# Optimization experiments

Measured on AMD Instinct MI355X. Metric: run time of the kernel, lower is better.

## Reference

```python
import jax, jax.numpy as jnp
import numpy as np

K_TOP = 2  # module's top-k


def setup_inputs() -> dict:
    key = jax.random.key(0)
    ks = jax.random.split(key, 6)
    s = 0.02
    B, S, H, D = 4, 1024, 2048, 1024
    E_SH, E_RT = 2, 16
    return {
        "x": jax.random.normal(ks[0], (B, S, H), dtype=jnp.float32),
        "Wsh_up": jax.random.normal(ks[1], (E_SH, H, D), dtype=jnp.float32) * s,
        "Wsh_down": jax.random.normal(ks[2], (E_SH, D, H), dtype=jnp.float32) * s,
        "Wrt_up": jax.random.normal(ks[3], (E_RT, H, D), dtype=jnp.float32) * s,
        "Wrt_down": jax.random.normal(ks[4], (E_RT, D, H), dtype=jnp.float32) * s,
        "W_router": jax.random.normal(ks[5], (H, E_RT), dtype=jnp.float32) * s,
    }


def reference(x, Wsh_up, Wsh_down, Wrt_up, Wrt_down, W_router):
    B, S, H = x.shape
    E_rt = Wrt_up.shape[0]
    xt = x.reshape(B * S, H)  # [T,H]

    # shared experts (summed)
    sh_mid = jax.nn.gelu(jnp.einsum('th,ehd->ted', xt, Wsh_up), approximate=False)
    shared_out = jnp.einsum('ted,edh->th', sh_mid, Wsh_down)  # [T,H]

    # router: softmax over all routed experts, then top-k
    probs = jax.nn.softmax(xt @ W_router, axis=-1)  # [T,E]
    top_v, top_i = jax.lax.top_k(probs, K_TOP)  # [T,K]
    # per-token dense gate weights over experts (zero for non-selected)
    gate = jnp.sum(jax.nn.one_hot(top_i, E_rt, dtype=xt.dtype) * top_v[..., None], axis=1)  # [T,E]

    # routed experts: compute all experts densely, combine with sparse gate
    rt_mid = jax.nn.gelu(jnp.einsum('th,ehd->ted', xt, Wrt_up), approximate=False)  # [T,E,D]
    routed_out = jnp.einsum('ted,edh->th', rt_mid * gate[:, :, None], Wrt_down)  # [T,H]

    return (shared_out + routed_out).reshape(B, S, H)
```

## Files before the change

### kernel.cpp

```cpp
#include <hip/hip_runtime.h>
#include <cstdint>
#include <cstddef>

typedef __bf16 bf16_t;
typedef __bf16 bf16x8 __attribute__((ext_vector_type(8)));
typedef float floatx4 __attribute__((ext_vector_type(4)));

static constexpr int T_TOK = 4096;
static constexpr int HDIM  = 2048;
static constexpr int DDIM  = 1024;
static constexpr int ESH   = 2;
static constexpr int ERT   = 16;
static constexpr int NPAIR = 2 * T_TOK;
static constexpr int NPAIR_PAD = NPAIR + 128;

__device__ __forceinline__ float gelu_f(float v) {
  return 0.5f * v * (1.0f + erff(v * 0.70710678118654752440f));
}

__global__ __launch_bounds__(256) void router_kernel(
    const float* __restrict__ x, const float* __restrict__ Wr,
    int* __restrict__ top_e, float* __restrict__ top_w, int* __restrict__ counts)
{
  const int t = blockIdx.x;
  const int tid = threadIdx.x;
  float acc[ERT];
#pragma unroll
  for (int e = 0; e < ERT; ++e) acc[e] = 0.f;
  const float* xr = x + (long)t * HDIM;
  for (int h = tid; h < HDIM; h += 256) {
    const float xv = xr[h];
    const float4* w4 = (const float4*)(Wr + h * ERT);
    const float4 w0 = w4[0], w1 = w4[1], w2 = w4[2], w3 = w4[3];
    acc[0]  += xv * w0.x; acc[1]  += xv * w0.y; acc[2]  += xv * w0.z; acc[3]  += xv * w0.w;
    acc[4]  += xv * w1.x; acc[5]  += xv * w1.y; acc[6]  += xv * w1.z; acc[7]  += xv * w1.w;
    acc[8]  += xv * w2.x; acc[9]  += xv * w2.y; acc[10] += xv * w2.z; acc[11] += xv * w2.w;
    acc[12] += xv * w3.x; acc[13] += xv * w3.y; acc[14] += xv * w3.z; acc[15] += xv * w3.w;
  }
  __shared__ float s[256][ERT + 1];
#pragma unroll
  for (int e = 0; e < ERT; ++e) s[tid][e] = acc[e];
  __syncthreads();
  for (int st = 128; st >= 1; st >>= 1) {
    if (tid < st) {
#pragma unroll
      for (int e = 0; e < ERT; ++e) s[tid][e] += s[tid + st][e];
    }
    __syncthreads();
  }
  if (tid == 0) {
    float l[ERT];
    float mx = -1e30f;
#pragma unroll
    for (int e = 0; e < ERT; ++e) { l[e] = s[0][e]; mx = fmaxf(mx, l[e]); }
    float sum = 0.f;
#pragma unroll
    for (int e = 0; e < ERT; ++e) { l[e] = expf(l[e] - mx); sum += l[e]; }
    const float inv = 1.f / sum;
    float v0 = -1.f, v1 = -1.f; int i0 = 0, i1 = 0;
#pragma unroll
    for (int e = 0; e < ERT; ++e) {
      const float p = l[e] * inv;
      if (p > v0) { v1 = v0; i1 = i0; v0 = p; i0 = e; }
      else if (p > v1) { v1 = p; i1 = e; }
    }
    top_e[2 * t] = i0; top_e[2 * t + 1] = i1;
    top_w[2 * t] = v0; top_w[2 * t + 1] = v1;
    atomicAdd(&counts[i0], 1); atomicAdd(&counts[i1], 1);
  }
}

__global__ void prefix_kernel(const int* __restrict__ counts, int* __restrict__ offsets) {
  if (threadIdx.x == 0) {
    int s = 0;
    for (int e = 0; e < ERT; ++e) { offsets[e] = s; s += counts[e]; }
    offsets[ERT] = s;
  }
}

__global__ __launch_bounds__(256) void scatter_kernel(
    const int* __restrict__ top_e, const float* __restrict__ top_w,
    const int* __restrict__ offsets, int* __restrict__ cursor,
    int* __restrict__ pair_token, float* __restrict__ pair_w)
{
  const int t = blockIdx.x * 256 + threadIdx.x;
  if (t >= T_TOK) return;
#pragma unroll
  for (int k = 0; k < 2; ++k) {
    const int e = top_e[2 * t + k];
    const int pos = atomicAdd(&cursor[e], 1);
    const int slot = offsets[e] + pos;
    pair_token[slot] = t;
    pair_w[slot] = top_w[2 * t + k];
  }
}

__global__ __launch_bounds__(256) void cast_x_kernel(const float* __restrict__ x, bf16_t* __restrict__ xb) {
  const long base = (long)blockIdx.x * HDIM + threadIdx.x * 8;
  const float4 a = *(const float4*)(x + base);
  const float4 b = *(const float4*)(x + base + 4);
  bf16x8 v;
  v[0] = (__bf16)a.x; v[1] = (__bf16)a.y; v[2] = (__bf16)a.z; v[3] = (__bf16)a.w;
  v[4] = (__bf16)b.x; v[5] = (__bf16)b.y; v[6] = (__bf16)b.z; v[7] = (__bf16)b.w;
  *(bf16x8*)(xb + base) = v;
}

__global__ __launch_bounds__(256) void gather_kernel(
    const float* __restrict__ x, const int* __restrict__ pair_token, bf16_t* __restrict__ xg)
{
  const int slot = blockIdx.x;
  const int tok = pair_token[slot];
  const float* src = x + (long)tok * HDIM;
  const int c = threadIdx.x * 8;
  const float4 a = *(const float4*)(src + c);
  const float4 b = *(const float4*)(src + c + 4);
  bf16x8 v;
  v[0] = (__bf16)a.x; v[1] = (__bf16)a.y; v[2] = (__bf16)a.z; v[3] = (__bf16)a.w;
  v[4] = (__bf16)b.x; v[5] = (__bf16)b.y; v[6] = (__bf16)b.z; v[7] = (__bf16)b.w;
  *(bf16x8*)(xg + (long)slot * HDIM + c) = v;
}

__global__ __launch_bounds__(256) void transpose_cast_kernel(
    const float* __restrict__ in, bf16_t* __restrict__ out, int R, int C)
{
  __shared__ float tl[64][65];
  const long mat = blockIdx.z;
  in  += mat * (long)R * C;
  out += mat * (long)R * C;
  const int c0 = blockIdx.x * 64, r0 = blockIdx.y * 64;
  const int tid = threadIdx.x;
  const int lr = tid >> 4;
  const int lc4 = (tid & 15) * 4;
#pragma unroll
  for (int i = 0; i < 4; ++i) {
    const int r = lr + i * 16;
    const float4 v = *(const float4*)(in + (long)(r0 + r) * C + c0 + lc4);
    tl[r][lc4 + 0] = v.x; tl[r][lc4 + 1] = v.y; tl[r][lc4 + 2] = v.z; tl[r][lc4 + 3] = v.w;
  }
  __syncthreads();
#pragma unroll
  for (int i = 0; i < 4; ++i) {
    const int c = lr + i * 16;
    ushort4 o;
    o.x = __builtin_bit_cast(unsigned short, (__bf16)tl[lc4 + 0][c]);
    o.y = __builtin_bit_cast(unsigned short, (__bf16)tl[lc4 + 1][c]);
    o.z = __builtin_bit_cast(unsigned short, (__bf16)tl[lc4 + 2][c]);
    o.w = __builtin_bit_cast(unsigned short, (__bf16)tl[lc4 + 3][c]);
    *(ushort4*)((unsigned short*)out + (long)(c0 + c) * R + r0 + lc4) = o;
  }
}

template<int MODE>
__global__ __launch_bounds__(256) void gemm_kernel(
    const bf16_t* __restrict__ Abase, const bf16_t* __restrict__ Bbase,
    bf16_t* __restrict__ Cbf, float* __restrict__ Cf,
    const int* __restrict__ counts, const int* __restrict__ offsets,
    const float* __restrict__ pair_w, const int* __restrict__ pair_token)
{
  constexpr int K   = (MODE == 3) ? 1024 : 2048;
  constexpr int LDA = (MODE == 3) ? 1024 : 2048;
  constexpr int LDB = (MODE == 1 || MODE == 3) ? 1024 : 2048;

  const int mt = blockIdx.x, nt = blockIdx.y, e = blockIdx.z;
  const int m0 = mt * 128;
  int cnt = 0, segoff = 0;
  if (MODE == 2 || MODE == 3) {
    cnt = counts[e];
    if (m0 >= cnt) return;
    segoff = offsets[e];
  }

  const bf16_t* Ab;
  const bf16_t* Bb;
  if (MODE == 0) {
    Ab = Abase + (long)m0 * LDA;
    Bb = Bbase + (long)(nt >> 3) * ((long)DDIM * HDIM) + (long)((nt & 7) * 128) * LDB;
  } else if (MODE == 1) {
    Ab = Abase + (long)m0 * LDA;
    Bb = Bbase + (long)(nt * 128) * LDB;
  } else if (MODE == 2) {
    Ab = Abase + (long)(segoff + m0) * LDA;
    Bb = Bbase + (long)e * ((long)DDIM * HDIM) + (long)(nt * 128) * LDB;
  } else {
    Ab = Abase + (long)(segoff + m0) * LDA;
    Bb = Bbase + (long)e * ((long)HDIM * DDIM) + (long)(nt * 128) * LDB;
  }

  __shared__ bf16_t As[128 * 72];
  __shared__ bf16_t Bs[128 * 72];

  const int tid = threadIdx.x;
  const int rr = tid >> 3, ch = tid & 7;
  const int lane = tid & 63, wv = tid >> 6;
  const int ln = lane & 15, quad = lane >> 4;
  const int wm = (wv & 1) * 64, wn = (wv >> 1) * 64;

  floatx4 acc[4][4];
#pragma unroll
  for (int i = 0; i < 4; ++i)
#pragma unroll
    for (int j = 0; j < 4; ++j) acc[i][j] = (floatx4){0.f, 0.f, 0.f, 0.f};

  for (int k0 = 0; k0 < K; k0 += 64) {
    bf16x8 av[4], bv[4];
    long bkoff;
    if (MODE == 1) bkoff = (long)(k0 >> 10) * ((long)HDIM * DDIM) + (k0 & 1023);
    else bkoff = k0;
#pragma unroll
    for (int i = 0; i < 4; ++i) {
      av[i] = *(const bf16x8*)(Ab + (long)(rr + i * 32) * LDA + k0 + ch * 8);
      bv[i] = *(const bf16x8*)(Bb + (long)(rr + i * 32) * LDB + bkoff + ch * 8);
    }
    __syncthreads();
#pragma unroll
    for (int i = 0; i < 4; ++i) {
      *(bf16x8*)(&As[(rr + i * 32) * 72 + ch * 8]) = av[i];
      *(bf16x8*)(&Bs[(rr + i * 32) * 72 + ch * 8]) = bv[i];
    }
    __syncthreads();
#pragma unroll
    for (int s = 0; s < 2; ++s) {
      bf16x8 af[4], bfr[4];
      const int ko = s * 32 + quad * 8;
#pragma unroll
      for (int mf = 0; mf < 4; ++mf) af[mf]  = *(const bf16x8*)(&As[(wm + mf * 16 + ln) * 72 + ko]);
#pragma unroll
      for (int nf = 0; nf < 4; ++nf) bfr[nf] = *(const bf16x8*)(&Bs[(wn + nf * 16 + ln) * 72 + ko]);
#pragma unroll
      for (int mf = 0; mf < 4; ++mf)
#pragma unroll
        for (int nf = 0; nf < 4; ++nf)
          acc[mf][nf] = __builtin_amdgcn_mfma_f32_16x16x32_bf16(af[mf], bfr[nf], acc[mf][nf], 0, 0, 0);
    }
  }

#pragma unroll
  for (int mf = 0; mf < 4; ++mf) {
#pragma unroll
    for (int r = 0; r < 4; ++r) {
      const int rl = wm + mf * 16 + quad * 4 + r;
      const int gm = m0 + rl;
      if ((MODE == 2 || MODE == 3) && gm >= cnt) continue;
      float wgt = 0.f; int tok = 0;
      if (MODE == 2) wgt = pair_w[segoff + gm];
      if (MODE == 3) tok = pair_token[segoff + gm];
#pragma unroll
      for (int nf = 0; nf < 4; ++nf) {
        const int clg = nt * 128 + wn + nf * 16 + ln;
        const float v = acc[mf][nf][r];
        if (MODE == 0)      Cbf[(long)gm * 2048 + clg] = (__bf16)gelu_f(v);
        else if (MODE == 1) Cf[(long)gm * 2048 + clg] = v;
        else if (MODE == 2) Cbf[(long)(segoff + gm) * 1024 + clg] = (__bf16)(gelu_f(v) * wgt);
        else                atomicAdd(&Cf[(long)tok * 2048 + clg], v);
      }
    }
  }
}

extern "C" void kernel_launch(void* const* d_in, const int* in_sizes, int n_in,
                              void* d_out, int out_size, void* d_ws, size_t ws_size,
                              hipStream_t stream)
{
  (void)in_sizes; (void)n_in; (void)out_size; (void)ws_size;
  const float* x        = (const float*)d_in[0];
  const float* Wsh_up   = (const float*)d_in[1];
  const float* Wsh_down = (const float*)d_in[2];
  const float* Wrt_up   = (const float*)d_in[3];
  const float* Wrt_down = (const float*)d_in[4];
  const float* Wr       = (const float*)d_in[5];
  float* out = (float*)d_out;

  char* w = (char*)d_ws;
  size_t off = 0;
  auto alloc = [&](size_t bytes) -> void* {
    void* p = w + off;
    off = (off + bytes + 255) & ~(size_t)255;
    return p;
  };
  int*    counts  = (int*)alloc(64);
  int*    cursor  = (int*)alloc(64);
  int*    offsets = (int*)alloc(128);
  int*    top_e   = (int*)alloc((size_t)2 * T_TOK * 4);
  float*  top_w   = (float*)alloc((size_t)2 * T_TOK * 4);
  int*    pair_token = (int*)alloc((size_t)NPAIR_PAD * 4);
  float*  pair_w  = (float*)alloc((size_t)NPAIR_PAD * 4);
  bf16_t* xb      = (bf16_t*)alloc((size_t)T_TOK * HDIM * 2);
  bf16_t* xg      = (bf16_t*)alloc((size_t)NPAIR_PAD * HDIM * 2);
  bf16_t* midsh   = (bf16_t*)alloc((size_t)T_TOK * (ESH * DDIM) * 2);
  bf16_t* midrt   = (bf16_t*)alloc((size_t)NPAIR_PAD * DDIM * 2);
  bf16_t* WshUt   = (bf16_t*)alloc((size_t)ESH * DDIM * HDIM * 2);
  bf16_t* WshDt   = (bf16_t*)alloc((size_t)ESH * HDIM * DDIM * 2);
  bf16_t* WrtUt   = (bf16_t*)alloc((size_t)ERT * DDIM * HDIM * 2);
  bf16_t* WrtDt   = (bf16_t*)alloc((size_t)ERT * HDIM * DDIM * 2);

  hipMemsetAsync(w, 0, 768, stream);

  router_kernel<<<T_TOK, 256, 0, stream>>>(x, Wr, top_e, top_w, counts);
  prefix_kernel<<<1, 64, 0, stream>>>(counts, offsets);
  scatter_kernel<<<T_TOK / 256, 256, 0, stream>>>(top_e, top_w, offsets, cursor, pair_token, pair_w);
  cast_x_kernel<<<T_TOK, 256, 0, stream>>>(x, xb);
  gather_kernel<<<NPAIR, 256, 0, stream>>>(x, pair_token, xg);

  transpose_cast_kernel<<<dim3(DDIM / 64, HDIM / 64, ESH), 256, 0, stream>>>(Wsh_up,   WshUt, HDIM, DDIM);
  transpose_cast_kernel<<<dim3(HDIM / 64, DDIM / 64, ESH), 256, 0, stream>>>(Wsh_down, WshDt, DDIM, HDIM);
  transpose_cast_kernel<<<dim3(DDIM / 64, HDIM / 64, ERT), 256, 0, stream>>>(Wrt_up,   WrtUt, HDIM, DDIM);
  transpose_cast_kernel<<<dim3(HDIM / 64, DDIM / 64, ERT), 256, 0, stream>>>(Wrt_down, WrtDt, DDIM, HDIM);

  gemm_kernel<0><<<dim3(32, 16, 1), 256, 0, stream>>>(xb, WshUt, midsh, nullptr,
                                                      nullptr, nullptr, nullptr, nullptr);
  gemm_kernel<2><<<dim3(32, 8, ERT), 256, 0, stream>>>(xg, WrtUt, midrt, nullptr,
                                                       counts, offsets, pair_w, nullptr);
  gemm_kernel<1><<<dim3(32, 16, 1), 256, 0, stream>>>(midsh, WshDt, nullptr, out,
                                                      nullptr, nullptr, nullptr, nullptr);
  gemm_kernel<3><<<dim3(32, 16, ERT), 256, 0, stream>>>(midrt, WrtDt, nullptr, out,
                                                        counts, offsets, nullptr, pair_token);
}
```

Baseline: 1.381 ms.

## Replace atomic scatter-add in down GEMMs with bf16 outputs and combine kernel

```diff
diff --git a/kernel.cpp b/kernel.cpp
--- a/kernel.cpp
+++ b/kernel.cpp
@@ -81,7 +81,8 @@
 __global__ __launch_bounds__(256) void scatter_kernel(
     const int* __restrict__ top_e, const float* __restrict__ top_w,
     const int* __restrict__ offsets, int* __restrict__ cursor,
-    int* __restrict__ pair_token, float* __restrict__ pair_w)
+    int* __restrict__ pair_token, float* __restrict__ pair_w,
+    int* __restrict__ inv_slot)
 {
   const int t = blockIdx.x * 256 + threadIdx.x;
   if (t >= T_TOK) return;
@@ -92,6 +93,7 @@
     const int slot = offsets[e] + pos;
     pair_token[slot] = t;
     pair_w[slot] = top_w[2 * t + k];
+    inv_slot[2 * t + k] = slot;
   }
 }
 
@@ -150,12 +152,35 @@
   }
 }
 
+__global__ __launch_bounds__(256) void combine_kernel(
+    const bf16_t* __restrict__ sh_out, const bf16_t* __restrict__ pair_out,
+    const int* __restrict__ inv_slot, float* __restrict__ out)
+{
+  const int t = blockIdx.x;
+  const int c = threadIdx.x * 8;
+  const int s0 = inv_slot[2 * t], s1 = inv_slot[2 * t + 1];
+  const bf16x8 a = *(const bf16x8*)(sh_out  + (long)t  * HDIM + c);
+  const bf16x8 b = *(const bf16x8*)(pair_out + (long)s0 * HDIM + c);
+  const bf16x8 d = *(const bf16x8*)(pair_out + (long)s1 * HDIM + c);
+  float4 o0, o1;
+  o0.x = (float)a[0] + (float)b[0] + (float)d[0];
+  o0.y = (float)a[1] + (float)b[1] + (float)d[1];
+  o0.z = (float)a[2] + (float)b[2] + (float)d[2];
+  o0.w = (float)a[3] + (float)b[3] + (float)d[3];
+  o1.x = (float)a[4] + (float)b[4] + (float)d[4];
+  o1.y = (float)a[5] + (float)b[5] + (float)d[5];
+  o1.z = (float)a[6] + (float)b[6] + (float)d[6];
+  o1.w = (float)a[7] + (float)b[7] + (float)d[7];
+  *(float4*)(out + (long)t * HDIM + c) = o0;
+  *(float4*)(out + (long)t * HDIM + c + 4) = o1;
+}
+
 template<int MODE>
 __global__ __launch_bounds__(256) void gemm_kernel(
     const bf16_t* __restrict__ Abase, const bf16_t* __restrict__ Bbase,
-    bf16_t* __restrict__ Cbf, float* __restrict__ Cf,
+    bf16_t* __restrict__ Cbf,
     const int* __restrict__ counts, const int* __restrict__ offsets,
-    const float* __restrict__ pair_w, const int* __restrict__ pair_token)
+    const float* __restrict__ pair_w)
 {
   constexpr int K   = (MODE == 3) ? 1024 : 2048;
   constexpr int LDA = (MODE == 3) ? 1024 : 2048;
@@ -241,17 +266,16 @@
       const int rl = wm + mf * 16 + quad * 4 + r;
       const int gm = m0 + rl;
       if ((MODE == 2 || MODE == 3) && gm >= cnt) continue;
-      float wgt = 0.f; int tok = 0;
+      float wgt = 0.f;
       if (MODE == 2) wgt = pair_w[segoff + gm];
-      if (MODE == 3) tok = pair_token[segoff + gm];
 #pragma unroll
       for (int nf = 0; nf < 4; ++nf) {
         const int clg = nt * 128 + wn + nf * 16 + ln;
         const float v = acc[mf][nf][r];
         if (MODE == 0)      Cbf[(long)gm * 2048 + clg] = (__bf16)gelu_f(v);
-        else if (MODE == 1) Cf[(long)gm * 2048 + clg] = v;
+        else if (MODE == 1) Cbf[(long)gm * 2048 + clg] = (__bf16)v;
         else if (MODE == 2) Cbf[(long)(segoff + gm) * 1024 + clg] = (__bf16)(gelu_f(v) * wgt);
-        else                atomicAdd(&Cf[(long)tok * 2048 + clg], v);
+        else                Cbf[(long)(segoff + gm) * 2048 + clg] = (__bf16)v;
       }
     }
   }
@@ -284,6 +308,7 @@
   float*  top_w   = (float*)alloc((size_t)2 * T_TOK * 4);
   int*    pair_token = (int*)alloc((size_t)NPAIR_PAD * 4);
   float*  pair_w  = (float*)alloc((size_t)NPAIR_PAD * 4);
+  int*    inv_slot = (int*)alloc((size_t)2 * T_TOK * 4);
   bf16_t* xb      = (bf16_t*)alloc((size_t)T_TOK * HDIM * 2);
   bf16_t* xg      = (bf16_t*)alloc((size_t)NPAIR_PAD * HDIM * 2);
   bf16_t* midsh   = (bf16_t*)alloc((size_t)T_TOK * (ESH * DDIM) * 2);
@@ -292,12 +317,15 @@
   bf16_t* WshDt   = (bf16_t*)alloc((size_t)ESH * HDIM * DDIM * 2);
   bf16_t* WrtUt   = (bf16_t*)alloc((size_t)ERT * DDIM * HDIM * 2);
   bf16_t* WrtDt   = (bf16_t*)alloc((size_t)ERT * HDIM * DDIM * 2);
+  bf16_t* sh_out   = xb;
+  bf16_t* pair_out = xg;
 
   hipMemsetAsync(w, 0, 768, stream);
 
   router_kernel<<<T_TOK, 256, 0, stream>>>(x, Wr, top_e, top_w, counts);
   prefix_kernel<<<1, 64, 0, stream>>>(counts, offsets);
-  scatter_kernel<<<T_TOK / 256, 256, 0, stream>>>(top_e, top_w, offsets, cursor, pair_token, pair_w);
+  scatter_kernel<<<T_TOK / 256, 256, 0, stream>>>(top_e, top_w, offsets, cursor,
+                                                  pair_token, pair_w, inv_slot);
   cast_x_kernel<<<T_TOK, 256, 0, stream>>>(x, xb);
   gather_kernel<<<NPAIR, 256, 0, stream>>>(x, pair_token, xg);
 
@@ -306,12 +334,13 @@
   transpose_cast_kernel<<<dim3(DDIM / 64, HDIM / 64, ERT), 256, 0, stream>>>(Wrt_up,   WrtUt, HDIM, DDIM);
   transpose_cast_kernel<<<dim3(HDIM / 64, DDIM / 64, ERT), 256, 0, stream>>>(Wrt_down, WrtDt, DDIM, HDIM);
 
-  gemm_kernel<0><<<dim3(32, 16, 1), 256, 0, stream>>>(xb, WshUt, midsh, nullptr,
-                                                      nullptr, nullptr, nullptr, nullptr);
-  gemm_kernel<2><<<dim3(32, 8, ERT), 256, 0, stream>>>(xg, WrtUt, midrt, nullptr,
-                                                       counts, offsets, pair_w, nullptr);
-  gemm_kernel<1><<<dim3(32, 16, 1), 256, 0, stream>>>(midsh, WshDt, nullptr, out,
-                                                      nullptr, nullptr, nullptr, nullptr);
-  gemm_kernel<3><<<dim3(32, 16, ERT), 256, 0, stream>>>(midrt, WrtDt, nullptr, out,
-                                                        counts, offsets, nullptr, pair_token);
-}
+  gemm_kernel<0><<<dim3(32, 16, 1), 256, 0, stream>>>(xb, WshUt, midsh,
+                                                      nullptr, nullptr, nullptr);
+  gemm_kernel<2><<<dim3(32, 8, ERT), 256, 0, stream>>>(xg, WrtUt, midrt,
+                                                       counts, offsets, pair_w);
+  gemm_kernel<1><<<dim3(32, 16, 1), 256, 0, stream>>>(midsh, WshDt, sh_out,
+                                                      nullptr, nullptr, nullptr);
+  gemm_kernel<3><<<dim3(32, 16, ERT), 256, 0, stream>>>(midrt, WrtDt, pair_out,
+                                                        counts, offsets, nullptr);
+  combine_kernel<<<T_TOK, 256, 0, stream>>>(sh_out, pair_out, inv_slot, out);
+}
```

New measurement: 1.241 ms. -10.2%, faster.
